# Kernel tuning notes

Measured on AMD Instinct MI355X. Metric: run time of the kernel, lower is better.

Reference implementation:

```python
import jax, jax.numpy as jnp
import numpy as np

B, N, C = 4, 4096, 128  # batch, tokens (flattened 3D volume), channels
F = 128  # filters


def setup_inputs() -> dict:
    key = jax.random.key(0)
    ks = jax.random.split(key, 7)
    s = 1.0 / np.sqrt(C)
    return {
        "inputs": jax.random.normal(ks[0], (B, N, C), dtype=jnp.float32),
        "Wq": jax.random.normal(ks[1], (C, F), dtype=jnp.float32) * s,
        "bq": jnp.zeros((F,), dtype=jnp.float32),
        "Wk": jax.random.normal(ks[2], (C, F), dtype=jnp.float32) * s,
        "bk": jnp.zeros((F,), dtype=jnp.float32),
        "Wv": jax.random.normal(ks[3], (C, F), dtype=jnp.float32) * s,
        "bv": jnp.zeros((F,), dtype=jnp.float32),
    }


def reference(inputs, Wq, bq, Wk, bk, Wv, bv):
    # Dense projections
    q = inputs @ Wq + bq  # [B, N, F]
    k = inputs @ Wk + bk
    v = inputs @ Wv + bv
    scale = jnp.sqrt(jnp.asarray(F, dtype=q.dtype))
    scores = jnp.einsum("bnf,bmf->bnm", q, k) / scale  # [B, N, N]
    weights = jax.nn.softmax(scores, axis=-1)
    return jnp.einsum("bnm,bmf->bnf", weights, v)
```

## Files before the change

### kernel.cpp

```cpp
#include <hip/hip_runtime.h>

typedef unsigned short u16;
typedef unsigned int u32;
typedef float f32x4 __attribute__((ext_vector_type(4)));
typedef short s16x8 __attribute__((ext_vector_type(8)));
typedef unsigned int u32x2 __attribute__((ext_vector_type(2)));
typedef unsigned int u32x4 __attribute__((ext_vector_type(4)));

#define NB 4
#define NT 4096
#define ND 128
#define NQ (NB * NT)

#define QK_SCALE 0.12751879523138906f

using as3_void = __attribute__((address_space(3))) void;
using as1_void = __attribute__((address_space(1))) void;

__device__ __forceinline__ u16 f2bf(float x){
  unsigned u = __float_as_uint(x);
  return (u16)((u + 0x7FFFu + ((u >> 16) & 1u)) >> 16);
}
__device__ __forceinline__ u32 cvtpk(float lo, float hi){
  u32 r; asm("v_cvt_pk_bf16_f32 %0, %1, %2" : "=v"(r) : "v"(lo), "v"(hi)); return r;
}
__device__ __forceinline__ f32x4 mfma16(s16x8 a, s16x8 b, f32x4 c){
  return __builtin_amdgcn_mfma_f32_16x16x32_bf16(a, b, c, 0, 0, 0);
}

__global__ void k_wprep(const float* __restrict__ Wq, const float* __restrict__ Wk,
                        const float* __restrict__ Wv, u16* __restrict__ WT){
  int mat = blockIdx.x >> 7;
  int f   = blockIdx.x & 127;
  const float* W = (mat == 0) ? Wq : (mat == 1) ? Wk : Wv;
  int c = threadIdx.x;
  WT[mat * 16384 + f * 128 + c] = f2bf(W[c * 128 + f]);
}

__global__ __launch_bounds__(256) void k_proj(
    const float* __restrict__ X, const u16* __restrict__ WT,
    const float* __restrict__ bq, const float* __restrict__ bk, const float* __restrict__ bv,
    u16* __restrict__ Qs, u16* __restrict__ Ks, u16* __restrict__ VTs)
{
  const int lane = threadIdx.x & 63;
  const int w    = threadIdx.x >> 6;
  const int lm = lane & 15, lg = lane >> 4;
  const int rowbase = blockIdx.x * 64 + w * 16;

  s16x8 a[4];
  const float* xr = X + (rowbase + lm) * ND;
  #pragma unroll
  for (int kc = 0; kc < 4; ++kc){
    f32x4 x0 = *(const f32x4*)(xr + kc * 32 + lg * 8);
    f32x4 x1 = *(const f32x4*)(xr + kc * 32 + lg * 8 + 4);
    s16x8 t;
    t[0]=(short)f2bf(x0[0]); t[1]=(short)f2bf(x0[1]); t[2]=(short)f2bf(x0[2]); t[3]=(short)f2bf(x0[3]);
    t[4]=(short)f2bf(x1[0]); t[5]=(short)f2bf(x1[1]); t[6]=(short)f2bf(x1[2]); t[7]=(short)f2bf(x1[3]);
    a[kc] = t;
  }

  #pragma unroll
  for (int mat = 0; mat < 3; ++mat){
    const float* bias = (mat==0) ? bq : (mat==1) ? bk : bv;
    float bl[8];
    #pragma unroll
    for (int n = 0; n < 8; ++n) bl[n] = bias[n * 16 + lm];
    f32x4 acc[8];
    #pragma unroll
    for (int n = 0; n < 8; ++n) acc[n] = f32x4{0.f,0.f,0.f,0.f};
    #pragma unroll
    for (int kc = 0; kc < 4; ++kc){
      #pragma unroll
      for (int n = 0; n < 8; ++n){
        s16x8 bf = *(const s16x8*)&WT[mat*16384 + (n*16 + lm)*128 + kc*32 + lg*8];
        acc[n] = mfma16(a[kc], bf, acc[n]);
      }
    }
    #pragma unroll
    for (int n = 0; n < 8; ++n){
      int f = n * 16 + lm;
      #pragma unroll
      for (int i = 0; i < 4; ++i){
        int r = rowbase + lg * 4 + i;
        float val = acc[n][i] + bl[n];
        if (mat == 0){
          Qs[r * ND + f] = f2bf(val * QK_SCALE);
        } else if (mat == 1){
          Ks[r * ND + (f ^ ((r & 7) << 3))] = f2bf(val);
        } else {
          int bb = r >> 12, nt = r & (NT - 1);
          VTs[(bb * ND + f) * NT + (nt ^ ((f & 3) << 3) ^ (((f >> 2) & 1) << 2))] = f2bf(val);
        }
      }
    }
  }
}

__global__ __launch_bounds__(512, 2) void k_attn(
    const u16* __restrict__ Qs, const u16* __restrict__ Ks,
    const u16* __restrict__ VTs, float* __restrict__ Out)
{
  __shared__ __align__(16) u16 lds[65536];
  u16* kbuf = lds;
  u16* vbuf = lds + 32768;

  const int lin = blockIdx.x;
  const int b   = (lin & 7) >> 1;
  const int qb  = (lin >> 3) + ((lin & 1) << 5);

  const int lane = threadIdx.x & 63;
  const int w  = threadIdx.x >> 6;
  const int g  = w >> 1, qw = w & 1;
  const int lm = lane & 15, lg = lane >> 4;
  const int q0 = b * NT + qb * 64 + qw * 32;

  s16x8 aq[2][4];
  #pragma unroll
  for (int sq = 0; sq < 2; ++sq){
    const u16* qr = Qs + (size_t)(q0 + sq * 16 + lm) * ND;
    #pragma unroll
    for (int kc = 0; kc < 4; ++kc) aq[sq][kc] = *(const s16x8*)(qr + kc * 32 + lg * 8);
  }

  f32x4 o[2][8];
  #pragma unroll
  for (int sq = 0; sq < 2; ++sq)
    #pragma unroll
    for (int n = 0; n < 8; ++n) o[sq][n] = f32x4{0.f,0.f,0.f,0.f};
  float l_[2] = {0.f, 0.f};

  const u16* gk = Ks  + ((size_t)b * NT + g * 1024 + qw * 16 + (lane >> 4)) * ND + (lane & 15) * 8;
  const u16* gv = VTs + ((size_t)b * ND + qw * 64 + (lane >> 2)) * NT + g * 1024 + (lane & 3) * 8;

  auto stage = [&](int par){
    u16* kd = kbuf + par * 16384 + g * 4096 + qw * 2048;
    u16* vd = vbuf + par * 16384 + g * 4096 + qw * 2048;
    #pragma unroll
    for (int j = 0; j < 4; ++j){
      __builtin_amdgcn_global_load_lds((const as1_void*)(gk + (size_t)j * 4 * ND),
                                       (as3_void*)(kd + j * 512), 16, 0, 0);
      __builtin_amdgcn_global_load_lds((const as1_void*)(gv + (size_t)j * 16 * NT),
                                       (as3_void*)(vd + j * 512), 16, 0, 0);
    }
    gk += (size_t)32 * ND;
    gv += 32;
  };

  stage(0);
  __syncthreads();
  int par = 0;

  const int kswz = (lm & 7) << 3;
  const int vswz = ((lm & 3) << 3) ^ (((lm >> 2) & 1) << 2);
  const int vcol0 = (lg * 4) ^ vswz;
  const int vcol1 = (16 + lg * 4) ^ vswz;

  for (int t = 0; t < 32; ++t){
    if (t < 31) stage(par ^ 1);
    const u16* kb = kbuf + par * 16384 + g * 4096;
    const u16* vb = vbuf + par * 16384 + g * 4096;

    f32x4 st[2][2];
    #pragma unroll
    for (int sq = 0; sq < 2; ++sq)
      #pragma unroll
      for (int n = 0; n < 2; ++n) st[sq][n] = f32x4{0.f,0.f,0.f,0.f};
    __builtin_amdgcn_s_setprio(1);
    #pragma unroll
    for (int kc = 0; kc < 4; ++kc){
      #pragma unroll
      for (int n = 0; n < 2; ++n){
        s16x8 kf = *(const s16x8*)&kb[(n * 16 + lm) * 128 + ((kc * 32 + lg * 8) ^ kswz)];
        st[0][n] = mfma16(kf, aq[0][kc], st[0][n]);
        st[1][n] = mfma16(kf, aq[1][kc], st[1][n]);
      }
    }
    __builtin_amdgcn_s_setprio(0);

    s16x8 pa[2];
    #pragma unroll
    for (int sq = 0; sq < 2; ++sq){
      float p[8];
      #pragma unroll
      for (int n = 0; n < 2; ++n)
        #pragma unroll
        for (int i = 0; i < 4; ++i){
          p[n * 4 + i] = __builtin_amdgcn_exp2f(st[sq][n][i]);
          l_[sq] += p[n * 4 + i];
        }
      pa[sq] = __builtin_bit_cast(s16x8, u32x4{
          cvtpk(p[0], p[1]), cvtpk(p[2], p[3]),
          cvtpk(p[4], p[5]), cvtpk(p[6], p[7])});
    }

    __builtin_amdgcn_s_setprio(1);
    #pragma unroll
    for (int nf = 0; nf < 8; ++nf){
      const int vr = (nf * 16 + lm) * 32;
      u32x2 v0 = *(const u32x2*)&vb[vr + vcol0];
      u32x2 v1 = *(const u32x2*)&vb[vr + vcol1];
      s16x8 vf = __builtin_bit_cast(s16x8, u32x4{v0[0], v0[1], v1[0], v1[1]});
      o[0][nf] = mfma16(pa[0], vf, o[0][nf]);
      o[1][nf] = mfma16(pa[1], vf, o[1][nf]);
    }
    __builtin_amdgcn_s_setprio(0);

    __syncthreads();
    par ^= 1;
  }

  #pragma unroll
  for (int sq = 0; sq < 2; ++sq){
    float v = l_[sq];
    v += __shfl_xor(v, 16);
    v += __shfl_xor(v, 32);
    l_[sq] = v;
  }

  float* mbF = (float*)lds;
  float* lF  = (float*)lds + 24576;
  __syncthreads();
  if (lg == 0){
    lF[g * 64 + qw * 32 + lm]      = l_[0];
    lF[g * 64 + qw * 32 + 16 + lm] = l_[1];
  }
  if (g){
    #pragma unroll
    for (int sq = 0; sq < 2; ++sq){
      #pragma unroll
      for (int i = 0; i < 4; ++i){
        const int row = (g - 1) * 64 + qw * 32 + sq * 16 + lg * 4 + i;
        #pragma unroll
        for (int nf = 0; nf < 8; ++nf)
          mbF[row * 128 + nf * 16 + lm] = o[sq][nf][i];
      }
    }
  }
  __syncthreads();
  if (!g){
    #pragma unroll
    for (int sq = 0; sq < 2; ++sq){
      #pragma unroll
      for (int i = 0; i < 4; ++i){
        const int rloc = qw * 32 + sq * 16 + lg * 4 + i;
        const float inv = 1.f / (lF[rloc] + lF[64 + rloc] + lF[128 + rloc] + lF[192 + rloc]);
        const size_t r = (size_t)(q0 + sq * 16 + lg * 4 + i);
        #pragma unroll
        for (int nf = 0; nf < 8; ++nf){
          const int f = nf * 16 + lm;
          float val = o[sq][nf][i] + mbF[rloc * 128 + f]
                    + mbF[(64 + rloc) * 128 + f] + mbF[(128 + rloc) * 128 + f];
          Out[r * ND + f] = val * inv;
        }
      }
    }
  }
}

extern "C" void kernel_launch(void* const* d_in, const int* in_sizes, int n_in,
                              void* d_out, int out_size, void* d_ws, size_t ws_size,
                              hipStream_t stream) {
  const float* X  = (const float*)d_in[0];
  const float* Wq = (const float*)d_in[1];
  const float* bq = (const float*)d_in[2];
  const float* Wk = (const float*)d_in[3];
  const float* bk = (const float*)d_in[4];
  const float* Wv = (const float*)d_in[5];
  const float* bv = (const float*)d_in[6];
  float* Out = (float*)d_out;

  u16* Qs  = (u16*)d_ws;
  u16* Ks  = Qs  + (size_t)NQ * ND;
  u16* VTs = Ks  + (size_t)NQ * ND;
  u16* WT  = VTs + (size_t)NQ * ND;

  hipLaunchKernelGGL(k_wprep, dim3(3 * 128), dim3(128), 0, stream, Wq, Wk, Wv, WT);
  hipLaunchKernelGGL(k_proj,  dim3(NQ / 64), dim3(256), 0, stream,
                     X, WT, bq, bk, bv, Qs, Ks, VTs);
  hipLaunchKernelGGL(k_attn,  dim3(256), dim3(512), 0, stream, Qs, Ks, VTs, Out);
}
```

Before: 79.24 us.

## Split KV range across blocks with 64-row query tiles and separate merge kernel

Each attention block now processes 128 queries (64 per wave pair) over half of the key/value sequence instead of 64 queries over all keys. This doubles reuse of each staged K/V tile across query rows and halves the loop count. Partial outputs and row sums are written to a workspace and combined by a new merge kernel that normalizes. The trade-offs are more accumulator registers, which may pressure occupancy, an extra kernel launch, and extra global traffic for the fp32 partials.

```diff
diff --git a/kernel.cpp b/kernel.cpp
--- a/kernel.cpp
+++ b/kernel.cpp
@@ -98,39 +98,43 @@
 
 __global__ __launch_bounds__(512, 2) void k_attn(
     const u16* __restrict__ Qs, const u16* __restrict__ Ks,
-    const u16* __restrict__ VTs, float* __restrict__ Out)
+    const u16* __restrict__ VTs, float* __restrict__ Op, float* __restrict__ lp)
 {
   __shared__ __align__(16) u16 lds[65536];
+  __shared__ float lbuf[2][2][64];
   u16* kbuf = lds;
   u16* vbuf = lds + 32768;
 
   const int lin = blockIdx.x;
-  const int b   = (lin & 7) >> 1;
-  const int qb  = (lin >> 3) + ((lin & 1) << 5);
+  const int logical = (lin & 7) * 32 + (lin >> 3);
+  const int qblk = logical & 127;
+  const int half = logical >> 7;
 
   const int lane = threadIdx.x & 63;
   const int w  = threadIdx.x >> 6;
   const int g  = w >> 1, qw = w & 1;
   const int lm = lane & 15, lg = lane >> 4;
-  const int q0 = b * NT + qb * 64 + qw * 32;
-
-  s16x8 aq[2][4];
-  #pragma unroll
-  for (int sq = 0; sq < 2; ++sq){
+  const int q0 = qblk * 128 + qw * 64;
+  const int b  = q0 >> 12;
+  const int kv0 = half * 2048 + g * 512;
+
+  s16x8 aq[4][4];
+  #pragma unroll
+  for (int sq = 0; sq < 4; ++sq){
     const u16* qr = Qs + (size_t)(q0 + sq * 16 + lm) * ND;
     #pragma unroll
     for (int kc = 0; kc < 4; ++kc) aq[sq][kc] = *(const s16x8*)(qr + kc * 32 + lg * 8);
   }
 
-  f32x4 o[2][8];
-  #pragma unroll
-  for (int sq = 0; sq < 2; ++sq)
+  f32x4 o[4][8];
+  #pragma unroll
+  for (int sq = 0; sq < 4; ++sq)
     #pragma unroll
     for (int n = 0; n < 8; ++n) o[sq][n] = f32x4{0.f,0.f,0.f,0.f};
-  float l_[2] = {0.f, 0.f};
-
-  const u16* gk = Ks  + ((size_t)b * NT + g * 1024 + qw * 16 + (lane >> 4)) * ND + (lane & 15) * 8;
-  const u16* gv = VTs + ((size_t)b * ND + qw * 64 + (lane >> 2)) * NT + g * 1024 + (lane & 3) * 8;
+  float l_[4] = {0.f, 0.f, 0.f, 0.f};
+
+  const u16* gk = Ks  + ((size_t)b * NT + kv0 + qw * 16 + (lane >> 4)) * ND + (lane & 15) * 8;
+  const u16* gv = VTs + ((size_t)b * ND + qw * 64 + (lane >> 2)) * NT + kv0 + (lane & 3) * 8;
 
   auto stage = [&](int par){
     u16* kd = kbuf + par * 16384 + g * 4096 + qw * 2048;
@@ -155,14 +159,14 @@
   const int vcol0 = (lg * 4) ^ vswz;
   const int vcol1 = (16 + lg * 4) ^ vswz;
 
-  for (int t = 0; t < 32; ++t){
-    if (t < 31) stage(par ^ 1);
+  for (int t = 0; t < 16; ++t){
+    if (t < 15) stage(par ^ 1);
     const u16* kb = kbuf + par * 16384 + g * 4096;
     const u16* vb = vbuf + par * 16384 + g * 4096;
 
-    f32x4 st[2][2];
-    #pragma unroll
-    for (int sq = 0; sq < 2; ++sq)
+    f32x4 st[4][2];
+    #pragma unroll
+    for (int sq = 0; sq < 4; ++sq)
       #pragma unroll
       for (int n = 0; n < 2; ++n) st[sq][n] = f32x4{0.f,0.f,0.f,0.f};
     __builtin_amdgcn_s_setprio(1);
@@ -171,15 +175,16 @@
       #pragma unroll
       for (int n = 0; n < 2; ++n){
         s16x8 kf = *(const s16x8*)&kb[(n * 16 + lm) * 128 + ((kc * 32 + lg * 8) ^ kswz)];
-        st[0][n] = mfma16(kf, aq[0][kc], st[0][n]);
-        st[1][n] = mfma16(kf, aq[1][kc], st[1][n]);
+        #pragma unroll
+        for (int sq = 0; sq < 4; ++sq)
+          st[sq][n] = mfma16(kf, aq[sq][kc], st[sq][n]);
       }
     }
     __builtin_amdgcn_s_setprio(0);
 
-    s16x8 pa[2];
-    #pragma unroll
-    for (int sq = 0; sq < 2; ++sq){
+    s16x8 pa[4];
+    #pragma unroll
+    for (int sq = 0; sq < 4; ++sq){
       float p[8];
       #pragma unroll
       for (int n = 0; n < 2; ++n)
@@ -200,8 +205,9 @@
       u32x2 v0 = *(const u32x2*)&vb[vr + vcol0];
       u32x2 v1 = *(const u32x2*)&vb[vr + vcol1];
       s16x8 vf = __builtin_bit_cast(s16x8, u32x4{v0[0], v0[1], v1[0], v1[1]});
-      o[0][nf] = mfma16(pa[0], vf, o[0][nf]);
-      o[1][nf] = mfma16(pa[1], vf, o[1][nf]);
+      #pragma unroll
+      for (int sq = 0; sq < 4; ++sq)
+        o[sq][nf] = mfma16(pa[sq], vf, o[sq][nf]);
     }
     __builtin_amdgcn_s_setprio(0);
 
@@ -210,7 +216,7 @@
   }
 
   #pragma unroll
-  for (int sq = 0; sq < 2; ++sq){
+  for (int sq = 0; sq < 4; ++sq){
     float v = l_[sq];
     v += __shfl_xor(v, 16);
     v += __shfl_xor(v, 32);
@@ -218,43 +224,80 @@
   }
 
   float* mbF = (float*)lds;
-  float* lF  = (float*)lds + 24576;
-  __syncthreads();
-  if (lg == 0){
-    lF[g * 64 + qw * 32 + lm]      = l_[0];
-    lF[g * 64 + qw * 32 + 16 + lm] = l_[1];
-  }
-  if (g){
-    #pragma unroll
-    for (int sq = 0; sq < 2; ++sq){
+  __syncthreads();
+  if (g >= 2){
+    float* dst = mbF + ((g - 2) * 2 + qw) * 8192;
+    #pragma unroll
+    for (int sq = 0; sq < 4; ++sq)
+      #pragma unroll
+      for (int i = 0; i < 4; ++i)
+        #pragma unroll
+        for (int nf = 0; nf < 8; ++nf)
+          dst[(sq * 16 + lg * 4 + i) * 128 + nf * 16 + lm] = o[sq][nf][i];
+    if (lg == 0){
+      #pragma unroll
+      for (int sq = 0; sq < 4; ++sq) lbuf[g - 2][qw][sq * 16 + lm] = l_[sq];
+    }
+  }
+  __syncthreads();
+  if (g < 2){
+    const float* src = mbF + (g * 2 + qw) * 8192;
+    #pragma unroll
+    for (int sq = 0; sq < 4; ++sq){
+      #pragma unroll
+      for (int i = 0; i < 4; ++i)
+        #pragma unroll
+        for (int nf = 0; nf < 8; ++nf)
+          o[sq][nf][i] += src[(sq * 16 + lg * 4 + i) * 128 + nf * 16 + lm];
+      l_[sq] += lbuf[g][qw][sq * 16 + lm];
+    }
+  }
+  __syncthreads();
+  if (g == 1){
+    float* dst = mbF + qw * 8192;
+    #pragma unroll
+    for (int sq = 0; sq < 4; ++sq)
+      #pragma unroll
+      for (int i = 0; i < 4; ++i)
+        #pragma unroll
+        for (int nf = 0; nf < 8; ++nf)
+          dst[(sq * 16 + lg * 4 + i) * 128 + nf * 16 + lm] = o[sq][nf][i];
+    if (lg == 0){
+      #pragma unroll
+      for (int sq = 0; sq < 4; ++sq) lbuf[0][qw][sq * 16 + lm] = l_[sq];
+    }
+  }
+  __syncthreads();
+  if (g == 0){
+    const float* src = mbF + qw * 8192;
+    #pragma unroll
+    for (int sq = 0; sq < 4; ++sq){
+      l_[sq] += lbuf[0][qw][sq * 16 + lm];
       #pragma unroll
       for (int i = 0; i < 4; ++i){
-        const int row = (g - 1) * 64 + qw * 32 + sq * 16 + lg * 4 + i;
+        const size_t r = (size_t)half * NQ + q0 + sq * 16 + lg * 4 + i;
         #pragma unroll
         for (int nf = 0; nf < 8; ++nf)
-          mbF[row * 128 + nf * 16 + lm] = o[sq][nf][i];
+          Op[r * ND + nf * 16 + lm] =
+              o[sq][nf][i] + src[(sq * 16 + lg * 4 + i) * 128 + nf * 16 + lm];
       }
-    }
-  }
-  __syncthreads();
-  if (!g){
-    #pragma unroll
-    for (int sq = 0; sq < 2; ++sq){
-      #pragma unroll
-      for (int i = 0; i < 4; ++i){
-        const int rloc = qw * 32 + sq * 16 + lg * 4 + i;
-        const float inv = 1.f / (lF[rloc] + lF[64 + rloc] + lF[128 + rloc] + lF[192 + rloc]);
-        const size_t r = (size_t)(q0 + sq * 16 + lg * 4 + i);
-        #pragma unroll
-        for (int nf = 0; nf < 8; ++nf){
-          const int f = nf * 16 + lm;
-          float val = o[sq][nf][i] + mbF[rloc * 128 + f]
-                    + mbF[(64 + rloc) * 128 + f] + mbF[(128 + rloc) * 128 + f];
-          Out[r * ND + f] = val * inv;
-        }
-      }
-    }
-  }
+      if (lg == 0) lp[(size_t)half * NQ + q0 + sq * 16 + lm] = l_[sq];
+    }
+  }
+}
+
+__global__ __launch_bounds__(256) void k_merge(const float* __restrict__ Op,
+                                               const float* __restrict__ lp,
+                                               float* __restrict__ Out){
+  const int gid = blockIdx.x * 256 + threadIdx.x;
+  const int q = gid >> 5, c = gid & 31;
+  f32x4 a = *(const f32x4*)(Op + (size_t)q * ND + c * 4);
+  f32x4 d = *(const f32x4*)(Op + ((size_t)NQ + q) * ND + c * 4);
+  const float inv = 1.f / (lp[q] + lp[NQ + q]);
+  f32x4 r;
+  r[0] = (a[0] + d[0]) * inv; r[1] = (a[1] + d[1]) * inv;
+  r[2] = (a[2] + d[2]) * inv; r[3] = (a[3] + d[3]) * inv;
+  *(f32x4*)(Out + (size_t)q * ND + c * 4) = r;
 }
 
 extern "C" void kernel_launch(void* const* d_in, const int* in_sizes, int n_in,
@@ -273,9 +316,12 @@
   u16* Ks  = Qs  + (size_t)NQ * ND;
   u16* VTs = Ks  + (size_t)NQ * ND;
   u16* WT  = VTs + (size_t)NQ * ND;
+  float* Op = (float*)(WT + 3 * 128 * 128);
+  float* lp = Op + (size_t)2 * NQ * ND;
 
   hipLaunchKernelGGL(k_wprep, dim3(3 * 128), dim3(128), 0, stream, Wq, Wk, Wv, WT);
   hipLaunchKernelGGL(k_proj,  dim3(NQ / 64), dim3(256), 0, stream,
                      X, WT, bq, bk, bv, Qs, Ks, VTs);
-  hipLaunchKernelGGL(k_attn,  dim3(256), dim3(512), 0, stream, Qs, Ks, VTs, Out);
-}
+  hipLaunchKernelGGL(k_attn,  dim3(256), dim3(512), 0, stream, Qs, Ks, VTs, Op, lp);
+  hipLaunchKernelGGL(k_merge, dim3(NQ * 32 / 256), dim3(256), 0, stream, Op, lp, Out);
+}
```

Measured after the change: 83.70 us. +5.6%, slower.

## Split KV across blocks with triple-buffered staging and separate merge kernel

Applied to the files above, without the earlier changes.

Each attention block now handles 128 queries over half the key range, with two wave groups splitting that half, instead of 64 queries over the full range with four groups. Partial outputs and row sums are written to workspace and combined by a new merge kernel. KV staging moves from double buffering with a full barrier to a three-deep ring, using explicit vmcnt waits and one barrier per iteration, which lets loads overlap compute. The cost is an extra kernel launch, extra global traffic for the partial outputs, and a larger workspace requirement.

```diff
diff --git a/kernel.cpp b/kernel.cpp
--- a/kernel.cpp
+++ b/kernel.cpp
@@ -98,21 +98,25 @@
 
 __global__ __launch_bounds__(512, 2) void k_attn(
     const u16* __restrict__ Qs, const u16* __restrict__ Ks,
-    const u16* __restrict__ VTs, float* __restrict__ Out)
+    const u16* __restrict__ VTs, float* __restrict__ Op, float* __restrict__ lp)
 {
-  __shared__ __align__(16) u16 lds[65536];
+  __shared__ __align__(16) u16 lds[49152];
+  __shared__ float lbuf[4][32];
   u16* kbuf = lds;
-  u16* vbuf = lds + 32768;
+  u16* vbuf = lds + 24576;
 
   const int lin = blockIdx.x;
-  const int b   = (lin & 7) >> 1;
-  const int qb  = (lin >> 3) + ((lin & 1) << 5);
+  const int logical = (lin & 7) * 32 + (lin >> 3);
+  const int qblk = logical & 127;
+  const int half = logical >> 7;
 
   const int lane = threadIdx.x & 63;
   const int w  = threadIdx.x >> 6;
-  const int g  = w >> 1, qw = w & 1;
+  const int g  = w & 1, qw = w >> 1;
   const int lm = lane & 15, lg = lane >> 4;
-  const int q0 = b * NT + qb * 64 + qw * 32;
+  const int q0 = qblk * 128 + qw * 32;
+  const int b  = q0 >> 12;
+  const int kv0 = half * 2048 + g * 1024;
 
   s16x8 aq[2][4];
   #pragma unroll
@@ -129,36 +133,47 @@
     for (int n = 0; n < 8; ++n) o[sq][n] = f32x4{0.f,0.f,0.f,0.f};
   float l_[2] = {0.f, 0.f};
 
-  const u16* gk = Ks  + ((size_t)b * NT + g * 1024 + qw * 16 + (lane >> 4)) * ND + (lane & 15) * 8;
-  const u16* gv = VTs + ((size_t)b * ND + qw * 64 + (lane >> 2)) * NT + g * 1024 + (lane & 3) * 8;
-
-  auto stage = [&](int par){
-    u16* kd = kbuf + par * 16384 + g * 4096 + qw * 2048;
-    u16* vd = vbuf + par * 16384 + g * 4096 + qw * 2048;
-    #pragma unroll
-    for (int j = 0; j < 4; ++j){
-      __builtin_amdgcn_global_load_lds((const as1_void*)(gk + (size_t)j * 4 * ND),
-                                       (as3_void*)(kd + j * 512), 16, 0, 0);
-      __builtin_amdgcn_global_load_lds((const as1_void*)(gv + (size_t)j * 16 * NT),
-                                       (as3_void*)(vd + j * 512), 16, 0, 0);
-    }
+  const u16* gk = Ks  + ((size_t)b * NT + kv0 + qw * 8 + (lane >> 4)) * ND + (lane & 15) * 8;
+  const u16* gv = VTs + ((size_t)b * ND + qw * 32 + (lane >> 2)) * NT + kv0 + (lane & 3) * 8;
+
+  auto stage = [&](int buf){
+    u16* kd = kbuf + (buf * 2 + g) * 4096 + qw * 1024;
+    u16* vd = vbuf + (buf * 2 + g) * 4096 + qw * 1024;
+    __builtin_amdgcn_global_load_lds((const as1_void*)gk,
+                                     (as3_void*)kd, 16, 0, 0);
+    __builtin_amdgcn_global_load_lds((const as1_void*)(gk + (size_t)4 * ND),
+                                     (as3_void*)(kd + 512), 16, 0, 0);
+    __builtin_amdgcn_global_load_lds((const as1_void*)gv,
+                                     (as3_void*)vd, 16, 0, 0);
+    __builtin_amdgcn_global_load_lds((const as1_void*)(gv + (size_t)16 * NT),
+                                     (as3_void*)(vd + 512), 16, 0, 0);
     gk += (size_t)32 * ND;
     gv += 32;
   };
-
-  stage(0);
-  __syncthreads();
-  int par = 0;
 
   const int kswz = (lm & 7) << 3;
   const int vswz = ((lm & 3) << 3) ^ (((lm >> 2) & 1) << 2);
   const int vcol0 = (lg * 4) ^ vswz;
   const int vcol1 = (16 + lg * 4) ^ vswz;
 
+  stage(0);
+  stage(1);
+  int bufr = 0, bufs = 2;
+
   for (int t = 0; t < 32; ++t){
-    if (t < 31) stage(par ^ 1);
-    const u16* kb = kbuf + par * 16384 + g * 4096;
-    const u16* vb = vbuf + par * 16384 + g * 4096;
+    if (t < 31) asm volatile("s_waitcnt vmcnt(4)" ::: "memory");
+    else        asm volatile("s_waitcnt vmcnt(0)" ::: "memory");
+    __builtin_amdgcn_sched_barrier(0);
+    __builtin_amdgcn_s_barrier();
+    __builtin_amdgcn_sched_barrier(0);
+
+    if (t < 30){
+      stage(bufs);
+      bufs = (bufs == 2) ? 0 : bufs + 1;
+    }
+
+    const u16* kb = kbuf + (bufr * 2 + g) * 4096;
+    const u16* vb = vbuf + (bufr * 2 + g) * 4096;
 
     f32x4 st[2][2];
     #pragma unroll
@@ -205,8 +220,7 @@
     }
     __builtin_amdgcn_s_setprio(0);
 
-    __syncthreads();
-    par ^= 1;
+    bufr = (bufr == 2) ? 0 : bufr + 1;
   }
 
   #pragma unroll
@@ -218,43 +232,48 @@
   }
 
   float* mbF = (float*)lds;
-  float* lF  = (float*)lds + 24576;
   __syncthreads();
-  if (lg == 0){
-    lF[g * 64 + qw * 32 + lm]      = l_[0];
-    lF[g * 64 + qw * 32 + 16 + lm] = l_[1];
-  }
-  if (g){
+  if (g == 1){
     #pragma unroll
     for (int sq = 0; sq < 2; ++sq){
       #pragma unroll
-      for (int i = 0; i < 4; ++i){
-        const int row = (g - 1) * 64 + qw * 32 + sq * 16 + lg * 4 + i;
+      for (int i = 0; i < 4; ++i)
         #pragma unroll
         for (int nf = 0; nf < 8; ++nf)
-          mbF[row * 128 + nf * 16 + lm] = o[sq][nf][i];
+          mbF[qw * 4096 + (sq * 16 + lg * 4 + i) * 128 + nf * 16 + lm] = o[sq][nf][i];
+      if (lg == 0) lbuf[qw][sq * 16 + lm] = l_[sq];
+    }
+  }
+  __syncthreads();
+  if (g == 0){
+    #pragma unroll
+    for (int sq = 0; sq < 2; ++sq){
+      l_[sq] += lbuf[qw][sq * 16 + lm];
+      #pragma unroll
+      for (int i = 0; i < 4; ++i){
+        const size_t r = (size_t)half * NQ + q0 + sq * 16 + lg * 4 + i;
+        #pragma unroll
+        for (int nf = 0; nf < 8; ++nf)
+          Op[r * ND + nf * 16 + lm] =
+              o[sq][nf][i] + mbF[qw * 4096 + (sq * 16 + lg * 4 + i) * 128 + nf * 16 + lm];
       }
-    }
-  }
-  __syncthreads();
-  if (!g){
-    #pragma unroll
-    for (int sq = 0; sq < 2; ++sq){
-      #pragma unroll
-      for (int i = 0; i < 4; ++i){
-        const int rloc = qw * 32 + sq * 16 + lg * 4 + i;
-        const float inv = 1.f / (lF[rloc] + lF[64 + rloc] + lF[128 + rloc] + lF[192 + rloc]);
-        const size_t r = (size_t)(q0 + sq * 16 + lg * 4 + i);
-        #pragma unroll
-        for (int nf = 0; nf < 8; ++nf){
-          const int f = nf * 16 + lm;
-          float val = o[sq][nf][i] + mbF[rloc * 128 + f]
-                    + mbF[(64 + rloc) * 128 + f] + mbF[(128 + rloc) * 128 + f];
-          Out[r * ND + f] = val * inv;
-        }
-      }
-    }
-  }
+      if (lg == 0) lp[(size_t)half * NQ + q0 + sq * 16 + lm] = l_[sq];
+    }
+  }
+}
+
+__global__ __launch_bounds__(256) void k_merge(const float* __restrict__ Op,
+                                               const float* __restrict__ lp,
+                                               float* __restrict__ Out){
+  const int gid = blockIdx.x * 256 + threadIdx.x;
+  const int q = gid >> 5, c = gid & 31;
+  f32x4 a = *(const f32x4*)(Op + (size_t)q * ND + c * 4);
+  f32x4 d = *(const f32x4*)(Op + ((size_t)NQ + q) * ND + c * 4);
+  const float inv = 1.f / (lp[q] + lp[NQ + q]);
+  f32x4 r;
+  r[0] = (a[0] + d[0]) * inv; r[1] = (a[1] + d[1]) * inv;
+  r[2] = (a[2] + d[2]) * inv; r[3] = (a[3] + d[3]) * inv;
+  *(f32x4*)(Out + (size_t)q * ND + c * 4) = r;
 }
 
 extern "C" void kernel_launch(void* const* d_in, const int* in_sizes, int n_in,
@@ -273,9 +292,12 @@
   u16* Ks  = Qs  + (size_t)NQ * ND;
   u16* VTs = Ks  + (size_t)NQ * ND;
   u16* WT  = VTs + (size_t)NQ * ND;
+  float* Op = (float*)(WT + 3 * 128 * 128);
+  float* lp = Op + (size_t)2 * NQ * ND;
 
   hipLaunchKernelGGL(k_wprep, dim3(3 * 128), dim3(128), 0, stream, Wq, Wk, Wv, WT);
   hipLaunchKernelGGL(k_proj,  dim3(NQ / 64), dim3(256), 0, stream,
                      X, WT, bq, bk, bv, Qs, Ks, VTs);
-  hipLaunchKernelGGL(k_attn,  dim3(256), dim3(512), 0, stream, Qs, Ks, VTs, Out);
-}
+  hipLaunchKernelGGL(k_attn,  dim3(256), dim3(512), 0, stream, Qs, Ks, VTs, Op, lp);
+  hipLaunchKernelGGL(k_merge, dim3(NQ * 32 / 256), dim3(256), 0, stream, Op, lp, Out);
+}
```

New measurement: 85.69 us. 8.1% more time.
